# Optimization experiments

Hardware: AMD Instinct MI355X
Metric: run time of the kernel (lower is better)

Reference implementation:

```python
import jax, jax.numpy as jnp
import numpy as np

N_NODES = 50000
N_REL = 4
N_EDGES = 250000
IN_F, HID_F, OUT_F = 512, 512, 256


def setup_inputs() -> dict:
    key = jax.random.key(0)
    ks = jax.random.split(key, 9)
    x = jax.random.normal(ks[0], (N_NODES, IN_F), dtype=jnp.float32)
    edge_src = jax.random.randint(ks[1], (N_REL, N_EDGES), 0, N_NODES, dtype=jnp.int64)
    edge_dst = jax.random.randint(ks[2], (N_REL, N_EDGES), 0, N_NODES, dtype=jnp.int64)
    s1 = 1.0 / np.sqrt(IN_F)
    s2 = 1.0 / np.sqrt(HID_F)
    Wself1 = jax.random.normal(ks[3], (N_REL, IN_F, HID_F), dtype=jnp.float32) * s1
    Wneigh1 = jax.random.normal(ks[4], (N_REL, IN_F, HID_F), dtype=jnp.float32) * s1
    b1 = jnp.zeros((N_REL, HID_F), dtype=jnp.float32)
    Wself2 = jax.random.normal(ks[5], (N_REL, HID_F, OUT_F), dtype=jnp.float32) * s2
    Wneigh2 = jax.random.normal(ks[6], (N_REL, HID_F, OUT_F), dtype=jnp.float32) * s2
    b2 = jnp.zeros((N_REL, OUT_F), dtype=jnp.float32)
    return {"x": x, "Wself1": Wself1, "Wneigh1": Wneigh1, "b1": b1,
            "Wself2": Wself2, "Wneigh2": Wneigh2, "b2": b2,
            "edge_src": edge_src, "edge_dst": edge_dst}


def _hetero_sage_layer(h, Wself, Wneigh, b, edge_src, edge_dst):
    """HeteroGraphConv(sum) over per-relation SAGEConv(mean) layers.

    DGL SAGEConv(mean): out_r = h @ W_self_r + mean_in_neigh(h) @ W_neigh_r + b_r;
    zero-in-degree nodes get a zero neighbor term (divide by max(deg,1)).
    """
    n = h.shape[0]
    out = jnp.zeros((n, Wself.shape[-1]), dtype=h.dtype)
    for r in range(Wself.shape[0]):  # small fixed number of relations
        src, dst = edge_src[r], edge_dst[r]
        deg = jax.ops.segment_sum(jnp.ones(src.shape, dtype=h.dtype), dst, num_segments=n)
        neigh_sum = jax.ops.segment_sum(h[src], dst, num_segments=n)  # [n, d]
        neigh = neigh_sum / jnp.maximum(deg, 1.0)[:, None]
        out = out + h @ Wself[r] + neigh @ Wneigh[r] + b[r]
    return out


def reference(x, Wself1, Wneigh1, b1, Wself2, Wneigh2, b2, edge_src, edge_dst):
    h = _hetero_sage_layer(x, Wself1, Wneigh1, b1, edge_src, edge_dst)
    h = jax.nn.relu(h)
    return _hetero_sage_layer(h, Wself2, Wneigh2, b2, edge_src, edge_dst)
```

## Files before the change

### kernel.cpp

```cpp
#include <hip/hip_runtime.h>
#include <stdint.h>

#define NNODES 50000
#define NREL 4
#define NEDGES 250000
#define INF 512
#define HIDF 512
#define OUTF 256
#define KCAT 2560
#define SCANB 49

typedef unsigned short u16;
typedef u16 u16x8 __attribute__((ext_vector_type(8)));
typedef __bf16 bf16x8 __attribute__((ext_vector_type(8)));
typedef float f32x4 __attribute__((ext_vector_type(4)));

__device__ __forceinline__ float bf2f(u16 b) {
    unsigned u = ((unsigned)b) << 16;
    return __builtin_bit_cast(float, u);
}
__device__ __forceinline__ u16 f2bf(float f) {
    unsigned u = __builtin_bit_cast(unsigned, f);
    u = (u + 0x7fffu + ((u >> 16) & 1u)) >> 16;
    return (u16)u;
}

#define GLOAD_LDS16(gsrc, ldst)                                                  \
    __builtin_amdgcn_global_load_lds(                                            \
        (__attribute__((address_space(1))) void*)(gsrc),                         \
        (__attribute__((address_space(3))) void*)(ldst), 16, 0, 0)


__global__ void cast_bf16_kernel(const float* __restrict__ in, u16* __restrict__ out, long total) {
    long i = ((long)blockIdx.x * blockDim.x + threadIdx.x) * 8;
    long stride = (long)gridDim.x * blockDim.x * 8;
    for (; i + 7 < total; i += stride) {
        float4 v0 = *(const float4*)(in + i);
        float4 v1 = *(const float4*)(in + i + 4);
        u16x8 o;
        o[0] = f2bf(v0.x); o[1] = f2bf(v0.y); o[2] = f2bf(v0.z); o[3] = f2bf(v0.w);
        o[4] = f2bf(v1.x); o[5] = f2bf(v1.y); o[6] = f2bf(v1.z); o[7] = f2bf(v1.w);
        *(u16x8*)(out + i) = o;
    }
}

__global__ void prep_weights_kernel(const float* __restrict__ Ws1, const float* __restrict__ Wn1,
                                    const float* __restrict__ Ws2, const float* __restrict__ Wn2,
                                    const float* __restrict__ b1, const float* __restrict__ b2,
                                    u16* __restrict__ WT1, u16* __restrict__ WT2,
                                    float* __restrict__ b1s, float* __restrict__ b2s) {
    const int T1 = HIDF * KCAT;
    const int T2 = OUTF * KCAT;
    const int total = T1 + T2 + HIDF + OUTF;
    for (int idx = blockIdx.x * blockDim.x + threadIdx.x; idx < total;
         idx += gridDim.x * blockDim.x) {
        if (idx < T1 + T2) {
            const float* Wself;
            const float* Wneigh;
            u16* WT;
            int N, id;
            if (idx < T1) { Wself = Ws1; Wneigh = Wn1; WT = WT1; N = HIDF; id = idx; }
            else          { Wself = Ws2; Wneigh = Wn2; WT = WT2; N = OUTF; id = idx - T1; }
            int n = id / KCAT;
            int kg = id - n * KCAT;
            int s = kg >> 9;
            int k = kg & 511;
            float v;
            if (s == 0) {
                v = Wself[(size_t)k * N + n] + Wself[(size_t)(512 + k) * N + n] +
                    Wself[(size_t)(1024 + k) * N + n] + Wself[(size_t)(1536 + k) * N + n];
            } else {
                v = Wneigh[((size_t)(s - 1) * 512 + k) * N + n];
            }
            WT[id] = f2bf(v);
        } else if (idx < T1 + T2 + HIDF) {
            int t = idx - T1 - T2;
            b1s[t] = b1[t] + b1[HIDF + t] + b1[2 * HIDF + t] + b1[3 * HIDF + t];
        } else {
            int t = idx - T1 - T2 - HIDF;
            b2s[t] = b2[t] + b2[OUTF + t] + b2[2 * OUTF + t] + b2[3 * OUTF + t];
        }
    }
}


__global__ void hist_kernel(const int* __restrict__ dst, int* __restrict__ deg) {
    int r = blockIdx.y;
    int i = blockIdx.x * blockDim.x + threadIdx.x;
    if (i < NEDGES) atomicAdd(&deg[r * NNODES + dst[r * NEDGES + i]], 1);
}

__global__ __launch_bounds__(1024) void scan1_kernel(const int* __restrict__ deg,
                                                     int* __restrict__ rp, int* __restrict__ bsum) {
    int rel = blockIdx.x / SCANB, blk = blockIdx.x % SCANB;
    int i = blk * 1024 + threadIdx.x;
    int v = (i < NNODES) ? deg[rel * NNODES + i] : 0;
    __shared__ int wsum[16];
    int lane = threadIdx.x & 63, wid = threadIdx.x >> 6;
    int x = v;
#pragma unroll
    for (int off = 1; off < 64; off <<= 1) {
        int o = __shfl_up(x, off);
        if (lane >= off) x += o;
    }
    if (lane == 63) wsum[wid] = x;
    __syncthreads();
    if (wid == 0) {
        int s = (lane < 16) ? wsum[lane] : 0;
#pragma unroll
        for (int off = 1; off < 16; off <<= 1) {
            int o = __shfl_up(s, off);
            if (lane >= off) s += o;
        }
        if (lane < 16) wsum[lane] = s;
    }
    __syncthreads();
    int excl = (wid > 0 ? wsum[wid - 1] : 0) + x - v;
    if (i < NNODES) rp[rel * (NNODES + 1) + i] = excl;
    if (threadIdx.x == 1023) bsum[blockIdx.x] = excl + v;
}

__global__ void scan2_kernel(const int* __restrict__ bsum, int* __restrict__ bofs) {
    int r = threadIdx.x >> 6, lane = threadIdx.x & 63;
    int v = (lane < SCANB) ? bsum[r * SCANB + lane] : 0;
    int x = v;
#pragma unroll
    for (int off = 1; off < 64; off <<= 1) {
        int o = __shfl_up(x, off);
        if (lane >= off) x += o;
    }
    if (lane < SCANB) bofs[r * SCANB + lane] = x - v;
}

__global__ __launch_bounds__(1024) void scan3_kernel(int* __restrict__ rp, int* __restrict__ cur,
                                                     const int* __restrict__ bofs) {
    int rel = blockIdx.x / SCANB, blk = blockIdx.x % SCANB;
    int i = blk * 1024 + threadIdx.x;
    if (i < NNODES) {
        int v = rp[rel * (NNODES + 1) + i] + bofs[rel * SCANB + blk];
        rp[rel * (NNODES + 1) + i] = v;
        cur[rel * NNODES + i] = v;
        if (i == 0) rp[rel * (NNODES + 1) + NNODES] = NEDGES;
    }
}

__global__ void fill_kernel(const int* __restrict__ esrc, const int* __restrict__ edst,
                            int* __restrict__ cur, int* __restrict__ col) {
    int r = blockIdx.y;
    int i = blockIdx.x * blockDim.x + threadIdx.x;
    if (i < NEDGES) {
        int d = edst[r * NEDGES + i];
        int pos = atomicAdd(&cur[r * NNODES + d], 1);
        col[r * NEDGES + pos] = esrc[r * NEDGES + i];
    }
}


__global__ __launch_bounds__(256) void aggregate_kernel(const u16* __restrict__ src,
                                                        const int* __restrict__ rp,
                                                        const int* __restrict__ col,
                                                        u16* __restrict__ out) {
    int node = blockIdx.x * 4 + (threadIdx.x >> 6);
    int rel = blockIdx.y;
    if (node >= NNODES) return;
    const int* r = rp + rel * (NNODES + 1);
    const int* cl = col + rel * NEDGES;
    int l = threadIdx.x & 63;
    int p0 = r[node], p1 = r[node + 1];
    int d = p1 - p0;
    float scale = (d > 0) ? 1.0f / (float)d : 1.0f;
    float acc[8] = {0.f, 0.f, 0.f, 0.f, 0.f, 0.f, 0.f, 0.f};
    const u16* srcl = src + l * 8;
    for (int base = 0; base < d; base += 64) {
        int ci = p0 + base + l;
        int myc = cl[ci < p1 ? ci : (p1 - 1)];
        int lim = d - base;
        if (lim > 64) lim = 64;
        int e = 0;
        for (; e + 4 <= lim; e += 4) {
            int s0 = __builtin_amdgcn_readlane(myc, e);
            int s1 = __builtin_amdgcn_readlane(myc, e + 1);
            int s2 = __builtin_amdgcn_readlane(myc, e + 2);
            int s3 = __builtin_amdgcn_readlane(myc, e + 3);
            u16x8 v0 = *(const u16x8*)(srcl + (size_t)s0 * 512);
            u16x8 v1 = *(const u16x8*)(srcl + (size_t)s1 * 512);
            u16x8 v2 = *(const u16x8*)(srcl + (size_t)s2 * 512);
            u16x8 v3 = *(const u16x8*)(srcl + (size_t)s3 * 512);
#pragma unroll
            for (int j = 0; j < 8; ++j)
                acc[j] += (bf2f(v0[j]) + bf2f(v1[j])) + (bf2f(v2[j]) + bf2f(v3[j]));
        }
        for (; e < lim; ++e) {
            int s0 = __builtin_amdgcn_readlane(myc, e);
            u16x8 v0 = *(const u16x8*)(srcl + (size_t)s0 * 512);
#pragma unroll
            for (int j = 0; j < 8; ++j) acc[j] += bf2f(v0[j]);
        }
    }
    u16x8 o;
#pragma unroll
    for (int j = 0; j < 8; ++j) o[j] = f2bf(acc[j] * scale);
    *(u16x8*)(out + ((size_t)rel * NNODES + node) * 512 + l * 8) = o;
}


template <int N, int OUTMODE>
__global__ __launch_bounds__(256, 4) void gemm_kernel(
    const u16* __restrict__ A0, const u16* __restrict__ A1, const u16* __restrict__ A2,
    const u16* __restrict__ A3, const u16* __restrict__ A4, const u16* __restrict__ WT,
    const float* __restrict__ bias, void* __restrict__ outp, int M) {
    __shared__ u16 ldsA[128 * 64];
    __shared__ u16 ldsB[128 * 64];
    const int t = threadIdx.x;
    const int w = t >> 6, l = t & 63;
    const int wr = w >> 1, wc = w & 1;

    constexpr int ncol = N >> 7;
    const int nwg = gridDim.x * gridDim.y;
    const int orig = blockIdx.y * gridDim.x + blockIdx.x;
    const int q = nwg >> 3, rr = nwg & 7, xcd = orig & 7, loc = orig >> 3;
    const int v = (xcd < rr) ? xcd * (q + 1) + loc : rr * (q + 1) + (xcd - rr) * q + loc;
    const int rowBase = (v / ncol) * 128;
    const int colBase = (v % ncol) * 128;

    f32x4 acc[4][4] = {};

    const u16* const As[5] = {A0, A1, A2, A3, A4};
    const int sr = t >> 3;
    const int gp = t & 7;
    const int lr = l & 15, lg = l >> 4;

#pragma unroll
    for (int s = 0; s < 5; ++s) {
        const u16* __restrict__ Asrc = As[s];
        for (int ts = 0; ts < 8; ++ts) {
            const int klocal = ts * 64;
            const int kglob = s * 512 + klocal;
#pragma unroll
            for (int c = 0; c < 4; ++c) {
                int r = c * 32 + sr;
                int gl = gp ^ (r & 7);
                int grow = rowBase + r;
                if (grow > M - 1) grow = M - 1;
                const u16* gsrc = Asrc + (size_t)grow * 512 + klocal + gl * 8;
                GLOAD_LDS16(gsrc, ldsA + (c * 2048 + w * 512));
            }
#pragma unroll
            for (int c = 0; c < 4; ++c) {
                int r = c * 32 + sr;
                int gl = gp ^ (r & 7);
                const u16* gsrc = WT + (size_t)(colBase + r) * KCAT + kglob + gl * 8;
                GLOAD_LDS16(gsrc, ldsB + (c * 2048 + w * 512));
            }
            __syncthreads();
#pragma unroll
            for (int kh = 0; kh < 2; ++kh) {
                bf16x8 av[4], bv[4];
#pragma unroll
                for (int m = 0; m < 4; ++m) {
                    int r = wr * 64 + m * 16 + lr;
                    int g = (kh * 4 + lg) ^ (r & 7);
                    av[m] = *(const bf16x8*)((const char*)ldsA + r * 128 + g * 16);
                }
#pragma unroll
                for (int n = 0; n < 4; ++n) {
                    int r = wc * 64 + n * 16 + lr;
                    int g = (kh * 4 + lg) ^ (r & 7);
                    bv[n] = *(const bf16x8*)((const char*)ldsB + r * 128 + g * 16);
                }
#pragma unroll
                for (int m = 0; m < 4; ++m)
#pragma unroll
                    for (int n = 0; n < 4; ++n)
                        acc[m][n] =
                            __builtin_amdgcn_mfma_f32_16x16x32_bf16(av[m], bv[n], acc[m][n], 0, 0, 0);
            }
            __syncthreads();
        }
    }

    const int lq = l >> 4;
#pragma unroll
    for (int m = 0; m < 4; ++m) {
#pragma unroll
        for (int n = 0; n < 4; ++n) {
#pragma unroll
            for (int j = 0; j < 4; ++j) {
                int row = rowBase + wr * 64 + m * 16 + lq * 4 + j;
                int colc = colBase + wc * 64 + n * 16 + lr;
                if (row < M) {
                    float vv = acc[m][n][j] + bias[colc];
                    if (OUTMODE == 0) {
                        vv = vv > 0.f ? vv : 0.f;
                        ((u16*)outp)[(size_t)row * N + colc] = f2bf(vv);
                    } else {
                        ((float*)outp)[(size_t)row * N + colc] = vv;
                    }
                }
            }
        }
    }
}


extern "C" void kernel_launch(void* const* d_in, const int* in_sizes, int n_in,
                              void* d_out, int out_size, void* d_ws, size_t ws_size,
                              hipStream_t stream) {
    const float* x = (const float*)d_in[0];
    const float* Wself1 = (const float*)d_in[1];
    const float* Wneigh1 = (const float*)d_in[2];
    const float* b1 = (const float*)d_in[3];
    const float* Wself2 = (const float*)d_in[4];
    const float* Wneigh2 = (const float*)d_in[5];
    const float* b2 = (const float*)d_in[6];
    const int* esrc = (const int*)d_in[7];
    const int* edst = (const int*)d_in[8];

    char* ws = (char*)d_ws;
    size_t off = 0;
    auto alloc = [&](size_t bytes) {
        char* p = ws + off;
        off += (bytes + 255) & ~(size_t)255;
        return p;
    };
    const size_t plane = (size_t)NNODES * 512;
    u16* xB = (u16*)alloc(plane * 2);
    u16* mB = (u16*)alloc(NREL * plane * 2);
    u16* h1B = (u16*)alloc(plane * 2);
    u16* WT1 = (u16*)alloc((size_t)HIDF * KCAT * 2);
    u16* WT2 = (u16*)alloc((size_t)OUTF * KCAT * 2);
    float* b1s = (float*)alloc(HIDF * 4);
    float* b2s = (float*)alloc(OUTF * 4);
    int* deg = (int*)alloc((size_t)NREL * NNODES * 4);
    int* rp = (int*)alloc((size_t)NREL * (NNODES + 1) * 4);
    int* cur = (int*)alloc((size_t)NREL * NNODES * 4);
    int* col = (int*)alloc((size_t)NREL * NEDGES * 4);
    int* bsum = (int*)alloc((size_t)NREL * SCANB * 4);
    int* bofs = (int*)alloc((size_t)NREL * SCANB * 4);

    hipMemsetAsync(deg, 0, (size_t)NREL * NNODES * 4, stream);
    cast_bf16_kernel<<<12500, 256, 0, stream>>>(x, xB, (long)NNODES * INF);
    prep_weights_kernel<<<1920, 256, 0, stream>>>(Wself1, Wneigh1, Wself2, Wneigh2,
                                                  b1, b2, WT1, WT2, b1s, b2s);
    hist_kernel<<<dim3(977, 4), 256, 0, stream>>>(edst, deg);
    scan1_kernel<<<NREL * SCANB, 1024, 0, stream>>>(deg, rp, bsum);
    scan2_kernel<<<1, 256, 0, stream>>>(bsum, bofs);
    scan3_kernel<<<NREL * SCANB, 1024, 0, stream>>>(rp, cur, bofs);
    fill_kernel<<<dim3(977, 4), 256, 0, stream>>>(esrc, edst, cur, col);

    aggregate_kernel<<<dim3(12500, 4), 256, 0, stream>>>(xB, rp, col, mB);
    gemm_kernel<HIDF, 0><<<dim3(4, 391), 256, 0, stream>>>(
        xB, mB, mB + plane, mB + 2 * plane, mB + 3 * plane, WT1, b1s, h1B, NNODES);

    aggregate_kernel<<<dim3(12500, 4), 256, 0, stream>>>(h1B, rp, col, mB);
    gemm_kernel<OUTF, 1><<<dim3(2, 391), 256, 0, stream>>>(
        h1B, mB, mB + plane, mB + 2 * plane, mB + 3 * plane, WT2, b2s, d_out, NNODES);
}
```

Measured before the change: 867.5 us.

## Tile weight transpose through LDS and widen aggregate gather to eight rows

The weight prep kernel now transposes 64x64 tiles through shared memory, so both the fp32 reads and the bf16 writes are coalesced instead of strided. Bias summing moves to its own tiny kernel. The neighbor aggregation loop now issues eight row gathers at a time, with masked weights for the tail, and folds the 1/deg scale into each accumulate, which removes the scalar remainder loop. This aims for more memory-level parallelism in the gather, at the cost of extra registers and wasted loads when a node has few neighbors.

```diff
diff --git a/kernel.cpp b/kernel.cpp
--- a/kernel.cpp
+++ b/kernel.cpp
@@ -44,43 +44,48 @@
     }
 }
 
-__global__ void prep_weights_kernel(const float* __restrict__ Ws1, const float* __restrict__ Wn1,
-                                    const float* __restrict__ Ws2, const float* __restrict__ Wn2,
-                                    const float* __restrict__ b1, const float* __restrict__ b2,
-                                    u16* __restrict__ WT1, u16* __restrict__ WT2,
-                                    float* __restrict__ b1s, float* __restrict__ b2s) {
-    const int T1 = HIDF * KCAT;
-    const int T2 = OUTF * KCAT;
-    const int total = T1 + T2 + HIDF + OUTF;
-    for (int idx = blockIdx.x * blockDim.x + threadIdx.x; idx < total;
-         idx += gridDim.x * blockDim.x) {
-        if (idx < T1 + T2) {
-            const float* Wself;
-            const float* Wneigh;
-            u16* WT;
-            int N, id;
-            if (idx < T1) { Wself = Ws1; Wneigh = Wn1; WT = WT1; N = HIDF; id = idx; }
-            else          { Wself = Ws2; Wneigh = Wn2; WT = WT2; N = OUTF; id = idx - T1; }
-            int n = id / KCAT;
-            int kg = id - n * KCAT;
-            int s = kg >> 9;
-            int k = kg & 511;
-            float v;
-            if (s == 0) {
-                v = Wself[(size_t)k * N + n] + Wself[(size_t)(512 + k) * N + n] +
-                    Wself[(size_t)(1024 + k) * N + n] + Wself[(size_t)(1536 + k) * N + n];
-            } else {
-                v = Wneigh[((size_t)(s - 1) * 512 + k) * N + n];
-            }
-            WT[id] = f2bf(v);
-        } else if (idx < T1 + T2 + HIDF) {
-            int t = idx - T1 - T2;
-            b1s[t] = b1[t] + b1[HIDF + t] + b1[2 * HIDF + t] + b1[3 * HIDF + t];
+__global__ __launch_bounds__(256) void prep_w_kernel(
+    const float* __restrict__ Ws1, const float* __restrict__ Wn1,
+    const float* __restrict__ Ws2, const float* __restrict__ Wn2,
+    u16* __restrict__ WT1, u16* __restrict__ WT2) {
+    __shared__ float tile[64][65];
+    int bid = blockIdx.x;
+    const float* Wself; const float* Wneigh; u16* WT;
+    int N, s, kt, nt;
+    if (bid < 320) {
+        N = HIDF; WT = WT1; Wself = Ws1; Wneigh = Wn1;
+        s = bid >> 6; int r = bid & 63; kt = r >> 3; nt = r & 7;
+    } else {
+        int b = bid - 320;
+        N = OUTF; WT = WT2; Wself = Ws2; Wneigh = Wn2;
+        s = b >> 5; int r = b & 31; kt = r >> 2; nt = r & 3;
+    }
+    int l = threadIdx.x & 63, wv = threadIdx.x >> 6;
+    int n0 = nt * 64 + l;
+    for (int i = 0; i < 16; ++i) {
+        int kl = wv + i * 4;
+        int k = kt * 64 + kl;
+        float v;
+        if (s == 0) {
+            v = Wself[(size_t)k * N + n0] + Wself[((size_t)512 + k) * N + n0] +
+                Wself[((size_t)1024 + k) * N + n0] + Wself[((size_t)1536 + k) * N + n0];
         } else {
-            int t = idx - T1 - T2 - HIDF;
-            b2s[t] = b2[t] + b2[OUTF + t] + b2[2 * OUTF + t] + b2[3 * OUTF + t];
-        }
-    }
+            v = Wneigh[((size_t)(s - 1) * 512 + k) * N + n0];
+        }
+        tile[kl][l] = v;
+    }
+    __syncthreads();
+    for (int i = 0; i < 16; ++i) {
+        int nl = wv + i * 4;
+        WT[(size_t)(nt * 64 + nl) * KCAT + s * 512 + kt * 64 + l] = f2bf(tile[l][nl]);
+    }
+}
+
+__global__ void prep_bias_kernel(const float* __restrict__ b1, const float* __restrict__ b2,
+                                 float* __restrict__ b1s, float* __restrict__ b2s) {
+    int t = threadIdx.x;
+    if (t < HIDF) b1s[t] = b1[t] + b1[HIDF + t] + b1[2 * HIDF + t] + b1[3 * HIDF + t];
+    if (t < OUTF) b2s[t] = b2[t] + b2[OUTF + t] + b2[2 * OUTF + t] + b2[3 * OUTF + t];
 }
 
 
@@ -176,30 +181,27 @@
         int myc = cl[ci < p1 ? ci : (p1 - 1)];
         int lim = d - base;
         if (lim > 64) lim = 64;
-        int e = 0;
-        for (; e + 4 <= lim; e += 4) {
-            int s0 = __builtin_amdgcn_readlane(myc, e);
-            int s1 = __builtin_amdgcn_readlane(myc, e + 1);
-            int s2 = __builtin_amdgcn_readlane(myc, e + 2);
-            int s3 = __builtin_amdgcn_readlane(myc, e + 3);
-            u16x8 v0 = *(const u16x8*)(srcl + (size_t)s0 * 512);
-            u16x8 v1 = *(const u16x8*)(srcl + (size_t)s1 * 512);
-            u16x8 v2 = *(const u16x8*)(srcl + (size_t)s2 * 512);
-            u16x8 v3 = *(const u16x8*)(srcl + (size_t)s3 * 512);
+        for (int e = 0; e < lim; e += 8) {
+            int idx[8]; float wgt[8];
+#pragma unroll
+            for (int j = 0; j < 8; ++j) {
+                int ee = e + j;
+                int lane = (ee < lim) ? ee : e;
+                idx[j] = __builtin_amdgcn_readlane(myc, lane);
+                wgt[j] = (ee < lim) ? scale : 0.0f;
+            }
+            u16x8 v[8];
+#pragma unroll
+            for (int j = 0; j < 8; ++j) v[j] = *(const u16x8*)(srcl + (size_t)idx[j] * 512);
 #pragma unroll
             for (int j = 0; j < 8; ++j)
-                acc[j] += (bf2f(v0[j]) + bf2f(v1[j])) + (bf2f(v2[j]) + bf2f(v3[j]));
-        }
-        for (; e < lim; ++e) {
-            int s0 = __builtin_amdgcn_readlane(myc, e);
-            u16x8 v0 = *(const u16x8*)(srcl + (size_t)s0 * 512);
-#pragma unroll
-            for (int j = 0; j < 8; ++j) acc[j] += bf2f(v0[j]);
+#pragma unroll
+                for (int f = 0; f < 8; ++f) acc[f] += wgt[j] * bf2f(v[j][f]);
         }
     }
     u16x8 o;
 #pragma unroll
-    for (int j = 0; j < 8; ++j) o[j] = f2bf(acc[j] * scale);
+    for (int j = 0; j < 8; ++j) o[j] = f2bf(acc[j]);
     *(u16x8*)(out + ((size_t)rel * NNODES + node) * 512 + l * 8) = o;
 }
 
@@ -340,8 +342,8 @@
 
     hipMemsetAsync(deg, 0, (size_t)NREL * NNODES * 4, stream);
     cast_bf16_kernel<<<12500, 256, 0, stream>>>(x, xB, (long)NNODES * INF);
-    prep_weights_kernel<<<1920, 256, 0, stream>>>(Wself1, Wneigh1, Wself2, Wneigh2,
-                                                  b1, b2, WT1, WT2, b1s, b2s);
+    prep_w_kernel<<<480, 256, 0, stream>>>(Wself1, Wneigh1, Wself2, Wneigh2, WT1, WT2);
+    prep_bias_kernel<<<1, 512, 0, stream>>>(b1, b2, b1s, b2s);
     hist_kernel<<<dim3(977, 4), 256, 0, stream>>>(edst, deg);
     scan1_kernel<<<NREL * SCANB, 1024, 0, stream>>>(deg, rp, bsum);
     scan2_kernel<<<1, 256, 0, stream>>>(bsum, bofs);
```

After: 843.4 us. 1.03x faster.
